# Kernel tuning notes

Hardware: AMD Instinct MI355X
Metric: run time of the kernel (lower is better)

## Reference

```python
import jax, jax.numpy as jnp
import numpy as np

B = 32          # batch_size
S = 64          # num_subgraph
D = 8           # dim_multi_hot (module-level global in source repo)
NE = S * D      # num_edges = 512
NNODES = 1024
E = 150000      # incidence rows
IN_UNITS = [16, 32, 32]
OUT_UNITS = [32, 32, 16]


def _glorot(key, shape):
    # glorot_normal over last two dims (out, in)
    fan_out, fan_in = shape[-2], shape[-1]
    std = (2.0 / (fan_in + fan_out)) ** 0.5
    return std * jax.random.normal(key, shape, dtype=jnp.float32)


def setup_inputs() -> dict:
    key = jax.random.key(0)
    ks = jax.random.split(key, 10)
    nodes_features = jax.random.normal(ks[0], (NNODES * S, IN_UNITS[0]), dtype=jnp.float32)
    c0 = jax.random.randint(ks[1], (E,), 0, B, dtype=jnp.int32)
    c1 = jax.random.randint(ks[2], (E,), 0, NNODES, dtype=jnp.int32)
    c2 = jax.random.randint(ks[3], (E,), 0, S, dtype=jnp.int32)
    c3 = jax.random.randint(ks[4], (E,), 0, D, dtype=jnp.int32)
    incidence_matrix = jnp.stack([c0, c1, c2, c3], axis=1)
    return {
        'nodes_features': nodes_features,
        'in_core0': _glorot(ks[5], (NE, IN_UNITS[1], IN_UNITS[0])),
        'in_bias0': jnp.zeros((NE, IN_UNITS[1], 1), jnp.float32),
        'in_core1': _glorot(ks[6], (NE, IN_UNITS[2], IN_UNITS[1])),
        'in_bias1': jnp.zeros((NE, IN_UNITS[2], 1), jnp.float32),
        'out_core0': _glorot(ks[7], (NE, OUT_UNITS[1], OUT_UNITS[0])),
        'out_bias0': jnp.zeros((NE, OUT_UNITS[1], 1), jnp.float32),
        'out_core1': _glorot(ks[8], (NE, OUT_UNITS[2], OUT_UNITS[1])),
        'out_bias1': jnp.zeros((NE, OUT_UNITS[2], 1), jnp.float32),
        'incidence_matrix': incidence_matrix,
    }


def reference(nodes_features, in_core0, in_bias0, in_core1, in_bias1,
              out_core0, out_bias0, out_core1, out_bias1, incidence_matrix):
    c0 = incidence_matrix[:, 0]
    c1 = incidence_matrix[:, 1]
    c2 = incidence_matrix[:, 2]
    c3 = incidence_matrix[:, 3]

    # gather node features per incidence row: [E, in0]
    x = nodes_features[c1 * S + c2]
    eidx = c2 * D + c3  # per-edge weight index, < NE

    # per-edge MLP (gathered batched matmul + bias + relu)
    for W, b in ((in_core0, in_bias0), (in_core1, in_bias1)):
        x = jax.nn.relu(jnp.einsum('eoi,ei->eo', W[eidx], x) + b[eidx, :, 0])

    # unsorted segment mean over irregular edge groups
    seg = c0 * (D * S) + c2 * D + c3
    nseg = B * S * D
    sums = jax.ops.segment_sum(x, seg, num_segments=nseg)           # [B*NE, 32]
    cnt = jax.ops.segment_sum(jnp.ones((x.shape[0], 1), x.dtype), seg, num_segments=nseg)
    ef = jnp.where(cnt > 0, sums / jnp.maximum(cnt, 1.0), 0.0)       # [B*NE, 32]

    # output MLP: weights tiled over batch (einsum avoids explicit repeat)
    ef = ef.reshape(B, NE, -1)
    for W, b in ((out_core0, out_bias0), (out_core1, out_bias1)):
        ef = jax.nn.relu(jnp.einsum('eoi,bei->beo', W, ef) + b[None, :, :, 0])

    return ef.reshape(B * NE, OUT_UNITS[-1], 1)
```

## Files before the change

### kernel.cpp

```cpp
#include <hip/hip_runtime.h>

#define B_    32
#define S_    64
#define D_    8
#define NE_   512
#define E_    150000
#define CAP   512


__global__ void zero_cursor(int* __restrict__ cursor) {
    cursor[threadIdx.x + blockIdx.x * 256] = 0;
}

__global__ __launch_bounds__(1024)
void scatter_kernel(const int* __restrict__ inc,
                    int* __restrict__ cursor,
                    int* __restrict__ payload) {
    __shared__ int lcount[NE_];
    __shared__ int lbase[NE_];
    const int tid = threadIdx.x;

    for (int i = tid; i < NE_; i += 1024) lcount[i] = 0;
    __syncthreads();

    const int e = blockIdx.x * 1024 + tid;
    int ei = -1, lp = 0, pl = 0;
    if (e < E_) {
        const int4 c = ((const int4*)inc)[e];
        ei = c.z * D_ + c.w;
        pl = (c.x << 16) | (c.y * S_ + c.z);
        lp = atomicAdd(&lcount[ei], 1);
    }
    __syncthreads();
    for (int i = tid; i < NE_; i += 1024) {
        const int c = lcount[i];
        lbase[i] = (c > 0) ? atomicAdd(&cursor[i], c) : 0;
    }
    __syncthreads();
    if (ei >= 0) {
        const int idx = lbase[ei] + lp;
        if (idx < CAP) payload[ei * CAP + idx] = pl;
    }
}

__global__ __launch_bounds__(512, 4)
void main_kernel(const float* __restrict__ nf,
                 const float* __restrict__ iw0, const float* __restrict__ ib0,
                 const float* __restrict__ iw1, const float* __restrict__ ib1,
                 const float* __restrict__ ow0, const float* __restrict__ ob0,
                 const float* __restrict__ ow1, const float* __restrict__ ob1,
                 const int* __restrict__ cursor, const int* __restrict__ payload,
                 float* __restrict__ out) {
    const int bid = blockIdx.x;
    const int tid = threadIdx.x;
    const int lane = tid & 63;
    const int wav  = tid >> 6;
    const int half = (tid >> 5) & 1;
    const int o    = lane & 31;
    const int slot_id = wav * 2 + half;

    __shared__ float hbuf[8][64];
    __shared__ float acc[32][33];
    __shared__ float hb[32][33];
    __shared__ float cnts[32];
    __shared__ __align__(16) float q0s[1024];
    __shared__ __align__(16) float q1s[512];
    __shared__ float qb0s[32], qb1s[16];

    float w0r[16], w1r[32];
    #pragma unroll
    for (int j = 0; j < 4; ++j) {
        float4 v = ((const float4*)(iw0 + (size_t)bid * 512 + o * 16))[j];
        w0r[4*j] = v.x; w0r[4*j+1] = v.y; w0r[4*j+2] = v.z; w0r[4*j+3] = v.w;
    }
    #pragma unroll
    for (int j = 0; j < 8; ++j) {
        float4 v = ((const float4*)(iw1 + (size_t)bid * 1024 + o * 32))[j];
        w1r[4*j] = v.x; w1r[4*j+1] = v.y; w1r[4*j+2] = v.z; w1r[4*j+3] = v.w;
    }
    float b0r = ib0[bid * 32 + o];
    float b1r = ib1[bid * 32 + o];
    #pragma unroll
    for (int k = 0; k < 16; ++k) asm volatile("" : "+v"(w0r[k]));
    #pragma unroll
    for (int k = 0; k < 32; ++k) asm volatile("" : "+v"(w1r[k]));
    asm volatile("" : "+v"(b0r));
    asm volatile("" : "+v"(b1r));

    for (int i = tid; i < 1024; i += 512) q0s[i] = ow0[(size_t)bid * 1024 + i];
    if (tid < 512) q1s[tid] = ow1[(size_t)bid * 512 + tid];
    if (tid < 32) { qb0s[tid] = ob0[bid * 32 + tid]; cnts[tid] = 0.f; }
    else if (tid < 48) qb1s[tid - 32] = ob1[bid * 16 + (tid - 32)];
    for (int i = tid; i < 32 * 33; i += 512) ((float*)acc)[i] = 0.f;
    __syncthreads();

    const int n = min(cursor[bid], CAP);
    for (int i = slot_id; i < n; i += 16) {
        const int p   = payload[bid * CAP + i];
        const int b   = p >> 16;
        const int row = p & 0xFFFF;

        float x[16];
        #pragma unroll
        for (int j = 0; j < 4; ++j) {
            float4 v = ((const float4*)(nf + (size_t)row * 16))[j];
            x[4*j] = v.x; x[4*j+1] = v.y; x[4*j+2] = v.z; x[4*j+3] = v.w;
        }
        float h = b0r;
        #pragma unroll
        for (int k = 0; k < 16; ++k) h = fmaf(w0r[k], x[k], h);
        h = fmaxf(h, 0.f);

        hbuf[wav][half * 32 + o] = h;
        __builtin_amdgcn_wave_barrier();
        float a = b1r;
        #pragma unroll
        for (int j = 0; j < 8; ++j) {
            float4 v = ((const float4*)&hbuf[wav][half * 32])[j];
            a = fmaf(w1r[4*j],   v.x, a); a = fmaf(w1r[4*j+1], v.y, a);
            a = fmaf(w1r[4*j+2], v.z, a); a = fmaf(w1r[4*j+3], v.w, a);
        }
        __builtin_amdgcn_wave_barrier();
        a = fmaxf(a, 0.f);

        atomicAdd(&acc[b][o], a);
        if (o == 0) atomicAdd(&cnts[b], 1.f);
    }
    __syncthreads();

    if (tid < 256) {
        const int b  = tid >> 3;
        const int o0 = (tid & 7) * 4;
        const float cv  = cnts[b];
        const float inv = cv > 0.f ? 1.0f / cv : 0.0f;
        #pragma unroll
        for (int j = 0; j < 4; ++j) {
            const int oo = o0 + j;
            float d = 0.f;
            #pragma unroll
            for (int k = 0; k < 32; ++k) d = fmaf(q0s[oo * 32 + k], acc[b][k], d);
            hb[b][oo] = fmaxf(fmaf(d, inv, qb0s[oo]), 0.f);
        }
    }
    __syncthreads();

    if (tid < 256) {
        const int b  = tid >> 3;
        const int o0 = (tid & 7) * 2;
        float r[2];
        #pragma unroll
        for (int j = 0; j < 2; ++j) {
            const int oo = o0 + j;
            float d = qb1s[oo];
            #pragma unroll
            for (int k = 0; k < 32; ++k) d = fmaf(q1s[oo * 32 + k], hb[b][k], d);
            r[j] = fmaxf(d, 0.f);
        }
        float2* op = (float2*)(out + ((size_t)b * NE_ + bid) * 16 + o0);
        *op = make_float2(r[0], r[1]);
    }
}

extern "C" void kernel_launch(void* const* d_in, const int* in_sizes, int n_in,
                              void* d_out, int out_size, void* d_ws, size_t ws_size,
                              hipStream_t stream) {
    const float* nf  = (const float*)d_in[0];
    const float* iw0 = (const float*)d_in[1];
    const float* ib0 = (const float*)d_in[2];
    const float* iw1 = (const float*)d_in[3];
    const float* ib1 = (const float*)d_in[4];
    const float* ow0 = (const float*)d_in[5];
    const float* ob0 = (const float*)d_in[6];
    const float* ow1 = (const float*)d_in[7];
    const float* ob1 = (const float*)d_in[8];
    const int*   inc = (const int*)d_in[9];

    int* cursor  = (int*)d_ws;
    int* payload = cursor + NE_;

    zero_cursor<<<2, 256, 0, stream>>>(cursor);
    scatter_kernel<<<(E_ + 1023) / 1024, 1024, 0, stream>>>(inc, cursor, payload);
    main_kernel<<<NE_, 512, 0, stream>>>(nf, iw0, ib0, iw1, ib1,
                                         ow0, ob0, ow1, ob1,
                                         cursor, payload, (float*)d_out);
}
```

Baseline: 128.9 us.

## Stage gathered node features as bf16 in scatter pass and prefetch in main kernel

The scatter kernel now gathers each incidence row's node features, converts them to bf16 and writes them contiguously per edge bucket, along with the batch index. The main kernel reads these staged features sequentially with one-iteration-ahead prefetching instead of doing random gathers into nf. This targets the latency of irregular gathers inside the per-edge loop. It costs extra workspace traffic and bf16 rounding of the inputs, and it keeps a fallback path for when the workspace is too small. A trailing wave barrier is also removed.

```diff
diff --git a/kernel.cpp b/kernel.cpp
--- a/kernel.cpp
+++ b/kernel.cpp
@@ -7,22 +7,211 @@
 #define E_    150000
 #define CAP   512
 
+#define BMETA_OFF   NE_
+#define XSTAGE_BYTE_OFF  (4 * (NE_ + NE_ * CAP))
+#define WS_NEED     (XSTAGE_BYTE_OFF + (size_t)NE_ * CAP * 16 * 2)
+
+__device__ __forceinline__ unsigned short f2bf(float f) {
+    union { float f; unsigned int u; } cv; cv.f = f;
+    unsigned int u = cv.u;
+    return (unsigned short)((u + 0x7fffu + ((u >> 16) & 1u)) >> 16);
+}
+__device__ __forceinline__ float bf2f(unsigned int u) {
+    union { unsigned int u; float f; } cv; cv.u = u << 16; return cv.f;
+}
 
 __global__ void zero_cursor(int* __restrict__ cursor) {
     cursor[threadIdx.x + blockIdx.x * 256] = 0;
 }
 
 __global__ __launch_bounds__(1024)
-void scatter_kernel(const int* __restrict__ inc,
-                    int* __restrict__ cursor,
+void scatter_stage_kernel(const int* __restrict__ inc,
+                          const float* __restrict__ nf,
+                          int* __restrict__ cursor,
+                          int* __restrict__ bmeta,
+                          uint4* __restrict__ xstage) {
+    __shared__ int lcount[NE_];
+    __shared__ int lbase[NE_];
+    const int tid = threadIdx.x;
+
+    for (int i = tid; i < NE_; i += 1024) lcount[i] = 0;
+    __syncthreads();
+
+    const int e = blockIdx.x * 1024 + tid;
+    int ei = -1, lp = 0, b = 0, row = 0;
+    if (e < E_) {
+        const int4 c = ((const int4*)inc)[e];
+        ei  = c.z * D_ + c.w;
+        b   = c.x;
+        row = c.y * S_ + c.z;
+        lp  = atomicAdd(&lcount[ei], 1);
+    }
+    __syncthreads();
+    for (int i = tid; i < NE_; i += 1024) {
+        const int c = lcount[i];
+        lbase[i] = (c > 0) ? atomicAdd(&cursor[i], c) : 0;
+    }
+    __syncthreads();
+    if (ei >= 0) {
+        const int idx = lbase[ei] + lp;
+        if (idx < CAP) {
+            const int slot = ei * CAP + idx;
+            bmeta[slot] = b;
+            const float4* xp = (const float4*)(nf + (size_t)row * 16);
+            float4 v0 = xp[0], v1 = xp[1], v2 = xp[2], v3 = xp[3];
+            uint4 pa, pb;
+            pa.x = f2bf(v0.x) | ((unsigned)f2bf(v0.y) << 16);
+            pa.y = f2bf(v0.z) | ((unsigned)f2bf(v0.w) << 16);
+            pa.z = f2bf(v1.x) | ((unsigned)f2bf(v1.y) << 16);
+            pa.w = f2bf(v1.z) | ((unsigned)f2bf(v1.w) << 16);
+            pb.x = f2bf(v2.x) | ((unsigned)f2bf(v2.y) << 16);
+            pb.y = f2bf(v2.z) | ((unsigned)f2bf(v2.w) << 16);
+            pb.z = f2bf(v3.x) | ((unsigned)f2bf(v3.y) << 16);
+            pb.w = f2bf(v3.z) | ((unsigned)f2bf(v3.w) << 16);
+            xstage[slot * 2]     = pa;
+            xstage[slot * 2 + 1] = pb;
+        }
+    }
+}
+
+__global__ __launch_bounds__(512, 4)
+void main_staged_kernel(const float* __restrict__ iw0, const float* __restrict__ ib0,
+                        const float* __restrict__ iw1, const float* __restrict__ ib1,
+                        const float* __restrict__ ow0, const float* __restrict__ ob0,
+                        const float* __restrict__ ow1, const float* __restrict__ ob1,
+                        const int* __restrict__ cursor, const int* __restrict__ bmeta,
+                        const uint4* __restrict__ xstage,
+                        float* __restrict__ out) {
+    const int bid = blockIdx.x;
+    const int tid = threadIdx.x;
+    const int lane = tid & 63;
+    const int wav  = tid >> 6;
+    const int half = (tid >> 5) & 1;
+    const int o    = lane & 31;
+    const int slot_id = wav * 2 + half;
+
+    __shared__ float hbuf[8][64];
+    __shared__ float acc[32][33];
+    __shared__ float hb[32][33];
+    __shared__ float cnts[32];
+    __shared__ __align__(16) float q0s[1024];
+    __shared__ __align__(16) float q1s[512];
+    __shared__ float qb0s[32], qb1s[16];
+
+    float w0r[16], w1r[32];
+    #pragma unroll
+    for (int j = 0; j < 4; ++j) {
+        float4 v = ((const float4*)(iw0 + (size_t)bid * 512 + o * 16))[j];
+        w0r[4*j] = v.x; w0r[4*j+1] = v.y; w0r[4*j+2] = v.z; w0r[4*j+3] = v.w;
+    }
+    #pragma unroll
+    for (int j = 0; j < 8; ++j) {
+        float4 v = ((const float4*)(iw1 + (size_t)bid * 1024 + o * 32))[j];
+        w1r[4*j] = v.x; w1r[4*j+1] = v.y; w1r[4*j+2] = v.z; w1r[4*j+3] = v.w;
+    }
+    float b0r = ib0[bid * 32 + o];
+    float b1r = ib1[bid * 32 + o];
+    #pragma unroll
+    for (int k = 0; k < 16; ++k) asm volatile("" : "+v"(w0r[k]));
+    #pragma unroll
+    for (int k = 0; k < 32; ++k) asm volatile("" : "+v"(w1r[k]));
+    asm volatile("" : "+v"(b0r));
+    asm volatile("" : "+v"(b1r));
+
+    for (int i = tid; i < 1024; i += 512) q0s[i] = ow0[(size_t)bid * 1024 + i];
+    if (tid < 512) q1s[tid] = ow1[(size_t)bid * 512 + tid];
+    if (tid < 32) { qb0s[tid] = ob0[bid * 32 + tid]; cnts[tid] = 0.f; }
+    else if (tid < 48) qb1s[tid - 32] = ob1[bid * 16 + (tid - 32)];
+    for (int i = tid; i < 32 * 33; i += 512) ((float*)acc)[i] = 0.f;
+    __syncthreads();
+
+    const int n = min(cursor[bid], CAP);
+    const uint4* Xs = xstage + (size_t)bid * CAP * 2;
+    const int*   Bm = bmeta + bid * CAP;
+
+    uint4 xa, xb; int bv = 0;
+    if (slot_id < n) {
+        xa = Xs[slot_id * 2]; xb = Xs[slot_id * 2 + 1]; bv = Bm[slot_id];
+    }
+    for (int i = slot_id; i < n; i += 16) {
+        const int inxt = i + 16;
+        uint4 xa2, xb2; int b2 = 0;
+        if (inxt < n) { xa2 = Xs[inxt * 2]; xb2 = Xs[inxt * 2 + 1]; b2 = Bm[inxt]; }
+
+        float x[16];
+        x[0]=bf2f(xa.x&0xffffu); x[1]=bf2f(xa.x>>16);
+        x[2]=bf2f(xa.y&0xffffu); x[3]=bf2f(xa.y>>16);
+        x[4]=bf2f(xa.z&0xffffu); x[5]=bf2f(xa.z>>16);
+        x[6]=bf2f(xa.w&0xffffu); x[7]=bf2f(xa.w>>16);
+        x[8]=bf2f(xb.x&0xffffu); x[9]=bf2f(xb.x>>16);
+        x[10]=bf2f(xb.y&0xffffu); x[11]=bf2f(xb.y>>16);
+        x[12]=bf2f(xb.z&0xffffu); x[13]=bf2f(xb.z>>16);
+        x[14]=bf2f(xb.w&0xffffu); x[15]=bf2f(xb.w>>16);
+
+        float h = b0r;
+        #pragma unroll
+        for (int k = 0; k < 16; ++k) h = fmaf(w0r[k], x[k], h);
+        h = fmaxf(h, 0.f);
+
+        hbuf[wav][half * 32 + o] = h;
+        __builtin_amdgcn_wave_barrier();
+        float a = b1r;
+        #pragma unroll
+        for (int j = 0; j < 8; ++j) {
+            float4 v = ((const float4*)&hbuf[wav][half * 32])[j];
+            a = fmaf(w1r[4*j],   v.x, a); a = fmaf(w1r[4*j+1], v.y, a);
+            a = fmaf(w1r[4*j+2], v.z, a); a = fmaf(w1r[4*j+3], v.w, a);
+        }
+        a = fmaxf(a, 0.f);
+
+        atomicAdd(&acc[bv][o], a);
+        if (o == 0) atomicAdd(&cnts[bv], 1.f);
+
+        xa = xa2; xb = xb2; bv = b2;
+    }
+    __syncthreads();
+
+    if (tid < 256) {
+        const int b  = tid >> 3;
+        const int o0 = (tid & 7) * 4;
+        const float cv  = cnts[b];
+        const float inv = cv > 0.f ? 1.0f / cv : 0.0f;
+        #pragma unroll
+        for (int j = 0; j < 4; ++j) {
+            const int oo = o0 + j;
+            float d = 0.f;
+            #pragma unroll
+            for (int k = 0; k < 32; ++k) d = fmaf(q0s[oo * 32 + k], acc[b][k], d);
+            hb[b][oo] = fmaxf(fmaf(d, inv, qb0s[oo]), 0.f);
+        }
+    }
+    __syncthreads();
+
+    if (tid < 256) {
+        const int b  = tid >> 3;
+        const int o0 = (tid & 7) * 2;
+        float r[2];
+        #pragma unroll
+        for (int j = 0; j < 2; ++j) {
+            const int oo = o0 + j;
+            float d = qb1s[oo];
+            #pragma unroll
+            for (int k = 0; k < 32; ++k) d = fmaf(q1s[oo * 32 + k], hb[b][k], d);
+            r[j] = fmaxf(d, 0.f);
+        }
+        float2* op = (float2*)(out + ((size_t)b * NE_ + bid) * 16 + o0);
+        *op = make_float2(r[0], r[1]);
+    }
+}
+
+__global__ __launch_bounds__(1024)
+void scatter_kernel(const int* __restrict__ inc, int* __restrict__ cursor,
                     int* __restrict__ payload) {
     __shared__ int lcount[NE_];
     __shared__ int lbase[NE_];
     const int tid = threadIdx.x;
-
     for (int i = tid; i < NE_; i += 1024) lcount[i] = 0;
     __syncthreads();
-
     const int e = blockIdx.x * 1024 + tid;
     int ei = -1, lp = 0, pl = 0;
     if (e < E_) {
@@ -99,7 +288,6 @@
         const int p   = payload[bid * CAP + i];
         const int b   = p >> 16;
         const int row = p & 0xFFFF;
-
         float x[16];
         #pragma unroll
         for (int j = 0; j < 4; ++j) {
@@ -110,7 +298,6 @@
         #pragma unroll
         for (int k = 0; k < 16; ++k) h = fmaf(w0r[k], x[k], h);
         h = fmaxf(h, 0.f);
-
         hbuf[wav][half * 32 + o] = h;
         __builtin_amdgcn_wave_barrier();
         float a = b1r;
@@ -120,9 +307,7 @@
             a = fmaf(w1r[4*j],   v.x, a); a = fmaf(w1r[4*j+1], v.y, a);
             a = fmaf(w1r[4*j+2], v.z, a); a = fmaf(w1r[4*j+3], v.w, a);
         }
-        __builtin_amdgcn_wave_barrier();
         a = fmaxf(a, 0.f);
-
         atomicAdd(&acc[b][o], a);
         if (o == 0) atomicAdd(&cnts[b], 1.f);
     }
@@ -143,7 +328,6 @@
         }
     }
     __syncthreads();
-
     if (tid < 256) {
         const int b  = tid >> 3;
         const int o0 = (tid & 7) * 2;
@@ -175,12 +359,22 @@
     const float* ob1 = (const float*)d_in[8];
     const int*   inc = (const int*)d_in[9];
 
-    int* cursor  = (int*)d_ws;
-    int* payload = cursor + NE_;
-
+    int* cursor = (int*)d_ws;
     zero_cursor<<<2, 256, 0, stream>>>(cursor);
-    scatter_kernel<<<(E_ + 1023) / 1024, 1024, 0, stream>>>(inc, cursor, payload);
-    main_kernel<<<NE_, 512, 0, stream>>>(nf, iw0, ib0, iw1, ib1,
-                                         ow0, ob0, ow1, ob1,
-                                         cursor, payload, (float*)d_out);
-}
+
+    if (ws_size >= WS_NEED) {
+        int*   bmeta  = cursor + BMETA_OFF;
+        uint4* xstage = (uint4*)((char*)d_ws + XSTAGE_BYTE_OFF);
+        scatter_stage_kernel<<<(E_ + 1023) / 1024, 1024, 0, stream>>>(
+            inc, nf, cursor, bmeta, xstage);
+        main_staged_kernel<<<NE_, 512, 0, stream>>>(
+            iw0, ib0, iw1, ib1, ow0, ob0, ow1, ob1,
+            cursor, bmeta, xstage, (float*)d_out);
+    } else {
+        int* payload = cursor + NE_;
+        scatter_kernel<<<(E_ + 1023) / 1024, 1024, 0, stream>>>(inc, cursor, payload);
+        main_kernel<<<NE_, 512, 0, stream>>>(nf, iw0, ib0, iw1, ib1,
+                                             ow0, ob0, ow1, ob1,
+                                             cursor, payload, (float*)d_out);
+    }
+}
```

New measurement: 134.8 us. 4.6% more time.

## Run per-edge MLP on bf16 MFMA with features pre-gathered during scatter

Applied to the files above, without the earlier changes.

The per-edge two-layer MLP now runs as bf16 32x32x16 MFMA tiles of 32 incidence rows, replacing per-thread scalar FMA loops. The scatter kernel now gathers each row's node features, packs them to bf16 and stages them with the batch id in edge-bucketed workspace, so the main kernel reads them contiguously. The cursor counters are padded to reduce atomic contention, zeroed with a memset, and the output-MLP weights are stored transposed in shared memory. The cost is bf16 rounding of inputs, weights and hidden activations, a lower per-edge capacity (CAP 448), and extra workspace traffic in the scatter stage.

```diff
diff --git a/kernel.cpp b/kernel.cpp
--- a/kernel.cpp
+++ b/kernel.cpp
@@ -5,17 +5,30 @@
 #define D_    8
 #define NE_   512
 #define E_    150000
-#define CAP   512
-
-
-__global__ void zero_cursor(int* __restrict__ cursor) {
-    cursor[threadIdx.x + blockIdx.x * 256] = 0;
+#define CAP   448
+#define CSTRIDE 16
+
+#define BMETA_BYTE_OFF   (NE_ * CSTRIDE * 4)
+#define XSTAGE_BYTE_OFF  (BMETA_BYTE_OFF + NE_ * CAP * 4)
+
+typedef __attribute__((ext_vector_type(8)))  short  short8;
+typedef __attribute__((ext_vector_type(16))) float  float16;
+
+__device__ __forceinline__ unsigned short f2bf(float f) {
+    union { float f; unsigned int u; } cv; cv.f = f;
+    unsigned int u = cv.u;
+    return (unsigned short)((u + 0x7fffu + ((u >> 16) & 1u)) >> 16);
+}
+__device__ __forceinline__ unsigned int pack2bf(float a, float b) {
+    return (unsigned int)f2bf(a) | ((unsigned int)f2bf(b) << 16);
 }
 
 __global__ __launch_bounds__(1024)
-void scatter_kernel(const int* __restrict__ inc,
-                    int* __restrict__ cursor,
-                    int* __restrict__ payload) {
+void scatter_stage_kernel(const int* __restrict__ inc,
+                          const float* __restrict__ nf,
+                          int* __restrict__ cursor,
+                          int* __restrict__ bmeta,
+                          uint4* __restrict__ xstage) {
     __shared__ int lcount[NE_];
     __shared__ int lbase[NE_];
     const int tid = threadIdx.x;
@@ -24,140 +37,170 @@
     __syncthreads();
 
     const int e = blockIdx.x * 1024 + tid;
-    int ei = -1, lp = 0, pl = 0;
+    int ei = -1, lp = 0, b = 0, row = 0;
     if (e < E_) {
         const int4 c = ((const int4*)inc)[e];
-        ei = c.z * D_ + c.w;
-        pl = (c.x << 16) | (c.y * S_ + c.z);
-        lp = atomicAdd(&lcount[ei], 1);
+        ei  = c.z * D_ + c.w;
+        b   = c.x;
+        row = c.y * S_ + c.z;
+        lp  = atomicAdd(&lcount[ei], 1);
     }
     __syncthreads();
     for (int i = tid; i < NE_; i += 1024) {
         const int c = lcount[i];
-        lbase[i] = (c > 0) ? atomicAdd(&cursor[i], c) : 0;
+        lbase[i] = (c > 0) ? atomicAdd(&cursor[i * CSTRIDE], c) : 0;
     }
     __syncthreads();
     if (ei >= 0) {
         const int idx = lbase[ei] + lp;
-        if (idx < CAP) payload[ei * CAP + idx] = pl;
-    }
-}
+        if (idx < CAP) {
+            const int slot = ei * CAP + idx;
+            bmeta[slot] = b;
+            const float4* xp = (const float4*)(nf + (size_t)row * 16);
+            float4 v0 = xp[0], v1 = xp[1], v2 = xp[2], v3 = xp[3];
+            uint4 pa, pb;
+            pa.x = pack2bf(v0.x, v0.y); pa.y = pack2bf(v0.z, v0.w);
+            pa.z = pack2bf(v1.x, v1.y); pa.w = pack2bf(v1.z, v1.w);
+            pb.x = pack2bf(v2.x, v2.y); pb.y = pack2bf(v2.z, v2.w);
+            pb.z = pack2bf(v3.x, v3.y); pb.w = pack2bf(v3.z, v3.w);
+            xstage[slot * 2]     = pa;
+            xstage[slot * 2 + 1] = pb;
+        }
+    }
+}
+
+#define HLP 40
 
 __global__ __launch_bounds__(512, 4)
-void main_kernel(const float* __restrict__ nf,
-                 const float* __restrict__ iw0, const float* __restrict__ ib0,
-                 const float* __restrict__ iw1, const float* __restrict__ ib1,
-                 const float* __restrict__ ow0, const float* __restrict__ ob0,
-                 const float* __restrict__ ow1, const float* __restrict__ ob1,
-                 const int* __restrict__ cursor, const int* __restrict__ payload,
-                 float* __restrict__ out) {
-    const int bid = blockIdx.x;
-    const int tid = threadIdx.x;
+void main_mfma(const float* __restrict__ iw0, const float* __restrict__ ib0,
+               const float* __restrict__ iw1, const float* __restrict__ ib1,
+               const float* __restrict__ ow0, const float* __restrict__ ob0,
+               const float* __restrict__ ow1, const float* __restrict__ ob1,
+               const int* __restrict__ cursor, const int* __restrict__ bmeta,
+               const uint4* __restrict__ xstage,
+               float* __restrict__ out) {
+    const int bid  = blockIdx.x;
+    const int tid  = threadIdx.x;
     const int lane = tid & 63;
     const int wav  = tid >> 6;
-    const int half = (tid >> 5) & 1;
-    const int o    = lane & 31;
-    const int slot_id = wav * 2 + half;
-
-    __shared__ float hbuf[8][64];
+    const int e32  = lane & 31;
+    const int q    = lane >> 5;
+
     __shared__ float acc[32][33];
     __shared__ float hb[32][33];
     __shared__ float cnts[32];
-    __shared__ __align__(16) float q0s[1024];
-    __shared__ __align__(16) float q1s[512];
+    __shared__ float q0t[32 * 33];
+    __shared__ float q1t[32 * 17];
     __shared__ float qb0s[32], qb1s[16];
-
-    float w0r[16], w1r[32];
+    __shared__ unsigned short Hl[8][32 * HLP];
+
+    short8 aWa, aWb0, aWb1;
+    {
+        const float* wa = iw0 + (size_t)bid * 512 + e32 * 16 + q * 8;
+        float4 u0 = ((const float4*)wa)[0], u1 = ((const float4*)wa)[1];
+        unsigned int p[4] = { pack2bf(u0.x,u0.y), pack2bf(u0.z,u0.w),
+                              pack2bf(u1.x,u1.y), pack2bf(u1.z,u1.w) };
+        aWa = *(short8*)p;
+    }
+    {
+        const float* wb = iw1 + (size_t)bid * 1024 + e32 * 32 + q * 8;
+        float4 u0 = ((const float4*)wb)[0], u1 = ((const float4*)wb)[1];
+        unsigned int p[4] = { pack2bf(u0.x,u0.y), pack2bf(u0.z,u0.w),
+                              pack2bf(u1.x,u1.y), pack2bf(u1.z,u1.w) };
+        aWb0 = *(short8*)p;
+        const float* wb2 = wb + 16;
+        float4 u2 = ((const float4*)wb2)[0], u3 = ((const float4*)wb2)[1];
+        unsigned int p2[4] = { pack2bf(u2.x,u2.y), pack2bf(u2.z,u2.w),
+                               pack2bf(u3.x,u3.y), pack2bf(u3.z,u3.w) };
+        aWb1 = *(short8*)p2;
+    }
+    float ba_r[16], bb_r[16];
     #pragma unroll
-    for (int j = 0; j < 4; ++j) {
-        float4 v = ((const float4*)(iw0 + (size_t)bid * 512 + o * 16))[j];
-        w0r[4*j] = v.x; w0r[4*j+1] = v.y; w0r[4*j+2] = v.z; w0r[4*j+3] = v.w;
-    }
-    #pragma unroll
-    for (int j = 0; j < 8; ++j) {
-        float4 v = ((const float4*)(iw1 + (size_t)bid * 1024 + o * 32))[j];
-        w1r[4*j] = v.x; w1r[4*j+1] = v.y; w1r[4*j+2] = v.z; w1r[4*j+3] = v.w;
-    }
-    float b0r = ib0[bid * 32 + o];
-    float b1r = ib1[bid * 32 + o];
-    #pragma unroll
-    for (int k = 0; k < 16; ++k) asm volatile("" : "+v"(w0r[k]));
-    #pragma unroll
-    for (int k = 0; k < 32; ++k) asm volatile("" : "+v"(w1r[k]));
-    asm volatile("" : "+v"(b0r));
-    asm volatile("" : "+v"(b1r));
-
-    for (int i = tid; i < 1024; i += 512) q0s[i] = ow0[(size_t)bid * 1024 + i];
-    if (tid < 512) q1s[tid] = ow1[(size_t)bid * 512 + tid];
+    for (int r = 0; r < 16; ++r) {
+        const int o_r = (r & 3) + 8 * (r >> 2) + 4 * q;
+        ba_r[r] = ib0[bid * 32 + o_r];
+        bb_r[r] = ib1[bid * 32 + o_r];
+    }
+
+    for (int i = tid; i < 1024; i += 512) {
+        const int o = i >> 5, k = i & 31;
+        q0t[k * 33 + o] = ow0[(size_t)bid * 1024 + i];
+    }
+    { const int o = tid >> 5, k = tid & 31;
+      q1t[k * 17 + o] = ow1[(size_t)bid * 512 + tid]; }
     if (tid < 32) { qb0s[tid] = ob0[bid * 32 + tid]; cnts[tid] = 0.f; }
     else if (tid < 48) qb1s[tid - 32] = ob1[bid * 16 + (tid - 32)];
     for (int i = tid; i < 32 * 33; i += 512) ((float*)acc)[i] = 0.f;
     __syncthreads();
 
-    const int n = min(cursor[bid], CAP);
-    for (int i = slot_id; i < n; i += 16) {
-        const int p   = payload[bid * CAP + i];
-        const int b   = p >> 16;
-        const int row = p & 0xFFFF;
-
-        float x[16];
-        #pragma unroll
-        for (int j = 0; j < 4; ++j) {
-            float4 v = ((const float4*)(nf + (size_t)row * 16))[j];
-            x[4*j] = v.x; x[4*j+1] = v.y; x[4*j+2] = v.z; x[4*j+3] = v.w;
-        }
-        float h = b0r;
-        #pragma unroll
-        for (int k = 0; k < 16; ++k) h = fmaf(w0r[k], x[k], h);
-        h = fmaxf(h, 0.f);
-
-        hbuf[wav][half * 32 + o] = h;
-        __builtin_amdgcn_wave_barrier();
-        float a = b1r;
-        #pragma unroll
-        for (int j = 0; j < 8; ++j) {
-            float4 v = ((const float4*)&hbuf[wav][half * 32])[j];
-            a = fmaf(w1r[4*j],   v.x, a); a = fmaf(w1r[4*j+1], v.y, a);
-            a = fmaf(w1r[4*j+2], v.z, a); a = fmaf(w1r[4*j+3], v.w, a);
-        }
-        __builtin_amdgcn_wave_barrier();
-        a = fmaxf(a, 0.f);
-
-        atomicAdd(&acc[b][o], a);
-        if (o == 0) atomicAdd(&cnts[b], 1.f);
-    }
-    __syncthreads();
-
-    if (tid < 256) {
-        const int b  = tid >> 3;
-        const int o0 = (tid & 7) * 4;
+    const int n = min(cursor[bid * CSTRIDE], CAP);
+    const int ntiles = (n + 31) >> 5;
+    const uint4* Xs = xstage + (size_t)bid * CAP * 2;
+    const int*   Bm = bmeta + bid * CAP;
+    unsigned short* hl = Hl[wav];
+
+    for (int t = wav; t < ntiles; t += 8) {
+        const int slot  = t * 32 + e32;
+        const bool valid = slot < n;
+        const int cs    = valid ? slot : (n - 1);
+
+        short8 bX = *(const short8*)&Xs[cs * 2 + q];
+        const int b_e = Bm[cs];
+
+        float16 c0;
+        #pragma unroll
+        for (int r = 0; r < 16; ++r) c0[r] = ba_r[r];
+        c0 = __builtin_amdgcn_mfma_f32_32x32x16_bf16(aWa, bX, c0, 0, 0, 0);
+
+        #pragma unroll
+        for (int r = 0; r < 16; r += 2) {
+            const int o_r = (r & 3) + 8 * (r >> 2) + 4 * q;
+            const unsigned int pk = pack2bf(fmaxf(c0[r], 0.f), fmaxf(c0[r + 1], 0.f));
+            *(unsigned int*)(hl + e32 * HLP + o_r) = pk;
+        }
+
+        short8 bH0 = *(const short8*)(hl + e32 * HLP + q * 8);
+        short8 bH1 = *(const short8*)(hl + e32 * HLP + 16 + q * 8);
+        float16 c1;
+        #pragma unroll
+        for (int r = 0; r < 16; ++r) c1[r] = bb_r[r];
+        c1 = __builtin_amdgcn_mfma_f32_32x32x16_bf16(aWb0, bH0, c1, 0, 0, 0);
+        c1 = __builtin_amdgcn_mfma_f32_32x32x16_bf16(aWb1, bH1, c1, 0, 0, 0);
+
+        if (valid) {
+            #pragma unroll
+            for (int r = 0; r < 16; ++r) {
+                const int o_r = (r & 3) + 8 * (r >> 2) + 4 * q;
+                atomicAdd(&acc[b_e][o_r], fmaxf(c1[r], 0.f));
+            }
+            if (q == 0) atomicAdd(&cnts[b_e], 1.f);
+        }
+    }
+    __syncthreads();
+
+    {
+        const int b  = tid >> 4;
+        const int j  = tid & 15;
         const float cv  = cnts[b];
         const float inv = cv > 0.f ? 1.0f / cv : 0.0f;
         #pragma unroll
-        for (int j = 0; j < 4; ++j) {
-            const int oo = o0 + j;
+        for (int s = 0; s < 2; ++s) {
+            const int oo = j * 2 + s;
             float d = 0.f;
             #pragma unroll
-            for (int k = 0; k < 32; ++k) d = fmaf(q0s[oo * 32 + k], acc[b][k], d);
+            for (int k = 0; k < 32; ++k) d = fmaf(q0t[k * 33 + oo], acc[b][k], d);
             hb[b][oo] = fmaxf(fmaf(d, inv, qb0s[oo]), 0.f);
         }
     }
     __syncthreads();
 
-    if (tid < 256) {
-        const int b  = tid >> 3;
-        const int o0 = (tid & 7) * 2;
-        float r[2];
-        #pragma unroll
-        for (int j = 0; j < 2; ++j) {
-            const int oo = o0 + j;
-            float d = qb1s[oo];
-            #pragma unroll
-            for (int k = 0; k < 32; ++k) d = fmaf(q1s[oo * 32 + k], hb[b][k], d);
-            r[j] = fmaxf(d, 0.f);
-        }
-        float2* op = (float2*)(out + ((size_t)b * NE_ + bid) * 16 + o0);
-        *op = make_float2(r[0], r[1]);
+    {
+        const int b = tid >> 4;
+        const int o = tid & 15;
+        float d = qb1s[o];
+        #pragma unroll
+        for (int k = 0; k < 32; ++k) d = fmaf(q1t[k * 17 + o], hb[b][k], d);
+        out[((size_t)b * NE_ + bid) * 16 + o] = fmaxf(d, 0.f);
     }
 }
 
@@ -175,12 +218,13 @@
     const float* ob1 = (const float*)d_in[8];
     const int*   inc = (const int*)d_in[9];
 
-    int* cursor  = (int*)d_ws;
-    int* payload = cursor + NE_;
-
-    zero_cursor<<<2, 256, 0, stream>>>(cursor);
-    scatter_kernel<<<(E_ + 1023) / 1024, 1024, 0, stream>>>(inc, cursor, payload);
-    main_kernel<<<NE_, 512, 0, stream>>>(nf, iw0, ib0, iw1, ib1,
-                                         ow0, ob0, ow1, ob1,
-                                         cursor, payload, (float*)d_out);
-}
+    int*   cursor = (int*)d_ws;
+    int*   bmeta  = (int*)((char*)d_ws + BMETA_BYTE_OFF);
+    uint4* xstage = (uint4*)((char*)d_ws + XSTAGE_BYTE_OFF);
+
+    hipMemsetAsync(cursor, 0, NE_ * CSTRIDE * 4, stream);
+    scatter_stage_kernel<<<(E_ + 1023) / 1024, 1024, 0, stream>>>(
+        inc, nf, cursor, bmeta, xstage);
+    main_mfma<<<NE_, 512, 0, stream>>>(iw0, ib0, iw1, ib1, ow0, ob0, ow1, ob1,
+                                       cursor, bmeta, xstage, (float*)d_out);
+}
```

New measurement: 123.9 us. 3.8% less time.
